# Performance work log

Measured on AMD Instinct MI355X. Metric: run time of the kernel, lower is better.

The kernel has to match this reference:

```python
import jax, jax.numpy as jnp
import numpy as np

E = 1024      # embed_dim
H = 16        # num_heads
HD = E // H   # head_dim = 64
M = 64        # num_landmarks


def setup_inputs() -> dict:
    key = jax.random.key(0)
    ks = jax.random.split(key, 9)
    B, Lq, Lk = 2, 2048, 2048
    inv = 1.0 / np.sqrt(E)
    return {
        "query": jax.random.normal(ks[0], (B, Lq, E), dtype=jnp.float32),
        "key":   jax.random.normal(ks[1], (B, Lk, E), dtype=jnp.float32),
        "value": jax.random.normal(ks[2], (B, Lk, E), dtype=jnp.float32),
        # learned params (xavier-ish scale)
        "Wv": jax.random.normal(ks[3], (E, E), dtype=jnp.float32) * inv,
        "bv": jnp.zeros((E,), dtype=jnp.float32),
        "Wl": jax.random.normal(ks[4], (M, E), dtype=jnp.float32) * inv,
        "bl": jnp.zeros((M,), dtype=jnp.float32),
        "Wo": jax.random.normal(ks[5], (E, E), dtype=jnp.float32) * inv,
        "bo": jnp.zeros((E,), dtype=jnp.float32),
    }


def reference(query, key, value, Wv, bv, Wl, bl, Wo, bo):
    B, Lq, _ = query.shape
    Lk = key.shape[1]
    # value projection -> [B, H, Lk, HD]
    v = (value @ Wv.T + bv).reshape(B, Lk, H, HD).transpose(0, 2, 1, 3)
    # landmark projections + softmax over landmark dim
    ql = jax.nn.softmax((query @ Wl.T + bl) / np.sqrt(M), axis=-1)  # [B, Lq, M]
    kl = jax.nn.softmax((key @ Wl.T + bl) / np.sqrt(M), axis=-1)    # [B, Lk, M]
    # landmark attention: [B, Lq, Lk], scaled by sqrt(head_dim), softmax over keys
    attn = jax.nn.softmax(
        jnp.einsum("bqm,bkm->bqk", ql, kl) / np.sqrt(HD), axis=-1)
    # apply shared attention across heads: [B, H, Lq, HD]
    out_h = jnp.einsum("bqk,bhkd->bhqd", attn, v)
    out = out_h.transpose(0, 2, 1, 3).reshape(B, Lq, E)
    return out @ Wo.T + bo
```

## Files before the change

kernel.cpp:

```cpp
#include <hip/hip_runtime.h>
#include <hip/hip_bf16.h>
#include <cstdint>

typedef unsigned short u16;
typedef __attribute__((ext_vector_type(8))) short short8;
typedef __attribute__((ext_vector_type(4))) float f32x4;
typedef __attribute__((ext_vector_type(4))) unsigned short us4;

__device__ __forceinline__ u16 f2bf(float f) {
    union { float f; unsigned int i; } v; v.f = f;
    unsigned int x = v.i;
    unsigned int r = x + 0x7fffu + ((x >> 16) & 1u);
    return (u16)(r >> 16);
}

enum { EPI_F32 = 0, EPI_BF16 = 1, EPI_EXP_RS = 3, EPI_F32_DIV_CB = 4, EPI_LMSM = 5 };

template <int BM, int BN, int EPI, bool AF32, bool BF32>
__device__ __forceinline__ void gemm_body(
    char* __restrict__ smem,
    const void* __restrict__ Ax, const void* __restrict__ A2x,
    const void* __restrict__ Bx, void* __restrict__ Cv,
    int M, int N, int K, long sA, long sB, long sC,
    const float* __restrict__ biasCol, float* __restrict__ rowScale, float expScale,
    int m0, int n0, int z)
{
    constexpr int BK = 64;
    constexpr int MFRAG = (BM + 31) / 32;
    constexpr int NFRAG = BN / 32;
    constexpr int AG = (BM + 31) / 32;
    constexpr int BG = BN / 32;
    constexpr int TBUF = (BM + BN) * BK;

    const int tid = threadIdx.x;
    const int lane = tid & 63;
    const int quad = lane >> 4;
    const int l15 = lane & 15;
    const int w = tid >> 6;
    const int wm = w >> 1, wn = w & 1;

    const int r8 = tid >> 3;
    const int cl = tid & 7;
    const int cg = ((cl ^ (r8 & 7)) * 8);

    const u16* ap[AG];
    const float* apf[AG];
    if constexpr (AF32) {
        const float* base = (const float*)Ax;
        long mr = m0;
        if (A2x != nullptr && m0 >= (M >> 1)) { base = (const float*)A2x; mr = m0 - (M >> 1); }
        const float* Afb = base + (long)z * sA + (long)mr * K;
#pragma unroll
        for (int j = 0; j < AG; ++j) apf[j] = Afb + (long)(j * 32 + r8) * K + cg;
    } else {
        const u16* Ab = (const u16*)Ax + (long)z * sA + (long)m0 * K;
#pragma unroll
        for (int j = 0; j < AG; ++j) ap[j] = Ab + (long)(j * 32 + r8) * K + cg;
    }
    const u16* bp[BG];
    const float* bpf[BG];
    if constexpr (BF32) {
        const float* Bfb = (const float*)Bx + (long)z * sB + (long)n0 * K;
#pragma unroll
        for (int j = 0; j < BG; ++j) bpf[j] = Bfb + (long)(j * 32 + r8) * K + cg;
    } else {
        const u16* Bb = (const u16*)Bx + (long)z * sB + (long)n0 * K;
#pragma unroll
        for (int j = 0; j < BG; ++j) bp[j] = Bb + (long)(j * 32 + r8) * K + cg;
    }

    f32x4 acc[MFRAG][NFRAG] = {};
    const int sw = l15 & 7;
    u16* const base16 = (u16*)smem;
    const int NT = K / BK;

    {
        u16* As = base16;
        u16* Bs = base16 + BM * BK;
        if constexpr (!AF32) {
#pragma unroll
            for (int j = 0; j < AG; ++j) {
                __builtin_amdgcn_global_load_lds(
                    (const __attribute__((address_space(1))) void*)(ap[j]),
                    (__attribute__((address_space(3))) void*)(&As[(j * 32 + r8) * BK + cl * 8]),
                    16, 0, 0);
                ap[j] += BK;
            }
        } else {
#pragma unroll
            for (int j = 0; j < AG; ++j) {
                const float4 u0 = *(const float4*)(apf[j]);
                const float4 u1 = *(const float4*)(apf[j] + 4);
                short8 o;
                o[0] = (short)f2bf(u0.x); o[1] = (short)f2bf(u0.y);
                o[2] = (short)f2bf(u0.z); o[3] = (short)f2bf(u0.w);
                o[4] = (short)f2bf(u1.x); o[5] = (short)f2bf(u1.y);
                o[6] = (short)f2bf(u1.z); o[7] = (short)f2bf(u1.w);
                *(short8*)&As[(j * 32 + r8) * BK + cl * 8] = o;
                apf[j] += BK;
            }
        }
        if constexpr (!BF32) {
#pragma unroll
            for (int j = 0; j < BG; ++j) {
                __builtin_amdgcn_global_load_lds(
                    (const __attribute__((address_space(1))) void*)(bp[j]),
                    (__attribute__((address_space(3))) void*)(&Bs[(j * 32 + r8) * BK + cl * 8]),
                    16, 0, 0);
                bp[j] += BK;
            }
        } else {
#pragma unroll
            for (int j = 0; j < BG; ++j) {
                const float4 u0 = *(const float4*)(bpf[j]);
                const float4 u1 = *(const float4*)(bpf[j] + 4);
                short8 o;
                o[0] = (short)f2bf(u0.x); o[1] = (short)f2bf(u0.y);
                o[2] = (short)f2bf(u0.z); o[3] = (short)f2bf(u0.w);
                o[4] = (short)f2bf(u1.x); o[5] = (short)f2bf(u1.y);
                o[6] = (short)f2bf(u1.z); o[7] = (short)f2bf(u1.w);
                *(short8*)&Bs[(j * 32 + r8) * BK + cl * 8] = o;
                bpf[j] += BK;
            }
        }
    }
    __syncthreads();

    for (int t = 0; t < NT; ++t) {
        u16* Asc = base16 + (t & 1) * TBUF;
        u16* Bsc = Asc + BM * BK;
        u16* Asn = base16 + ((t + 1) & 1) * TBUF;
        u16* Bsn = Asn + BM * BK;
        const bool pf = (t + 1 < NT);

        float4 ra[AG][2];
        float4 rb[BG][2];
        if (pf) {
            if constexpr (!AF32) {
#pragma unroll
                for (int j = 0; j < AG; ++j) {
                    __builtin_amdgcn_global_load_lds(
                        (const __attribute__((address_space(1))) void*)(ap[j]),
                        (__attribute__((address_space(3))) void*)(&Asn[(j * 32 + r8) * BK + cl * 8]),
                        16, 0, 0);
                    ap[j] += BK;
                }
            } else {
#pragma unroll
                for (int j = 0; j < AG; ++j) {
                    ra[j][0] = *(const float4*)(apf[j]);
                    ra[j][1] = *(const float4*)(apf[j] + 4);
                    apf[j] += BK;
                }
            }
            if constexpr (!BF32) {
#pragma unroll
                for (int j = 0; j < BG; ++j) {
                    __builtin_amdgcn_global_load_lds(
                        (const __attribute__((address_space(1))) void*)(bp[j]),
                        (__attribute__((address_space(3))) void*)(&Bsn[(j * 32 + r8) * BK + cl * 8]),
                        16, 0, 0);
                    bp[j] += BK;
                }
            } else {
#pragma unroll
                for (int j = 0; j < BG; ++j) {
                    rb[j][0] = *(const float4*)(bpf[j]);
                    rb[j][1] = *(const float4*)(bpf[j] + 4);
                    bpf[j] += BK;
                }
            }
        }

#pragma unroll
        for (int ks = 0; ks < 2; ++ks) {
            short8 af[MFRAG], bfr[NFRAG];
#pragma unroll
            for (int i = 0; i < MFRAG; ++i)
                af[i] = *(const short8*)&Asc[(wm * (BM / 2) + i * 16 + l15) * BK +
                                             (((ks * 4 + quad) ^ sw) * 8)];
#pragma unroll
            for (int i = 0; i < NFRAG; ++i)
                bfr[i] = *(const short8*)&Bsc[(wn * (BN / 2) + i * 16 + l15) * BK +
                                              (((ks * 4 + quad) ^ sw) * 8)];
#pragma unroll
            for (int i = 0; i < MFRAG; ++i)
#pragma unroll
                for (int jn = 0; jn < NFRAG; ++jn)
                    acc[i][jn] = __builtin_amdgcn_mfma_f32_16x16x32_bf16(af[i], bfr[jn], acc[i][jn], 0, 0, 0);
        }

        if (pf) {
            if constexpr (AF32) {
#pragma unroll
                for (int j = 0; j < AG; ++j) {
                    short8 o;
                    o[0] = (short)f2bf(ra[j][0].x); o[1] = (short)f2bf(ra[j][0].y);
                    o[2] = (short)f2bf(ra[j][0].z); o[3] = (short)f2bf(ra[j][0].w);
                    o[4] = (short)f2bf(ra[j][1].x); o[5] = (short)f2bf(ra[j][1].y);
                    o[6] = (short)f2bf(ra[j][1].z); o[7] = (short)f2bf(ra[j][1].w);
                    *(short8*)&Asn[(j * 32 + r8) * BK + cl * 8] = o;
                }
            }
            if constexpr (BF32) {
#pragma unroll
                for (int j = 0; j < BG; ++j) {
                    short8 o;
                    o[0] = (short)f2bf(rb[j][0].x); o[1] = (short)f2bf(rb[j][0].y);
                    o[2] = (short)f2bf(rb[j][0].z); o[3] = (short)f2bf(rb[j][0].w);
                    o[4] = (short)f2bf(rb[j][1].x); o[5] = (short)f2bf(rb[j][1].y);
                    o[6] = (short)f2bf(rb[j][1].z); o[7] = (short)f2bf(rb[j][1].w);
                    *(short8*)&Bsn[(j * 32 + r8) * BK + cl * 8] = o;
                }
            }
        }
        __syncthreads();
    }

    if constexpr (EPI == EPI_LMSM) {
        float* red = (float*)(base16 + 2 * TBUF);
        float ev[4][NFRAG];
#pragma unroll
        for (int r = 0; r < 4; ++r) {
            float s = 0.f;
#pragma unroll
            for (int jn = 0; jn < NFRAG; ++jn) {
                const int col = wn * (BN / 2) + jn * 16 + l15;
                float v = exp2f((acc[0][jn][r] + biasCol[col]) * expScale);
                ev[r][jn] = v; s += v;
            }
            s += __shfl_xor(s, 1); s += __shfl_xor(s, 2);
            s += __shfl_xor(s, 4); s += __shfl_xor(s, 8);
            if (l15 == 0) red[wn * BM + wm * 16 + quad * 4 + r] = s;
        }
        __syncthreads();
#pragma unroll
        for (int r = 0; r < 4; ++r) {
            const int mrow = wm * 16 + quad * 4 + r;
            const float inv = 1.0f / (red[mrow] + red[BM + mrow]);
            const long m = m0 + mrow;
#pragma unroll
            for (int jn = 0; jn < NFRAG; ++jn) {
                const int col = wn * (BN / 2) + jn * 16 + l15;
                ((u16*)Cv)[m * N + col] = f2bf(ev[r][jn] * inv);
            }
        }
        return;
    } else {
#pragma unroll
        for (int i = 0; i < MFRAG; ++i) {
            const int mb = m0 + wm * (BM / 2) + i * 16 + quad * 4;
#pragma unroll
            for (int r = 0; r < 4; ++r) {
                const int m = mb + r;
                float rin = 0.f;
                if constexpr (EPI == EPI_F32_DIV_CB) rin = 1.0f / rowScale[(long)z * M + m];
                float rowsum = 0.f;
#pragma unroll
                for (int jn = 0; jn < NFRAG; ++jn) {
                    const int col = n0 + wn * (BN / 2) + jn * 16 + l15;
                    float v = acc[i][jn][r];
                    if constexpr (EPI == EPI_EXP_RS) { v = exp2f(v * expScale); rowsum += v; }
                    if constexpr (EPI == EPI_F32_DIV_CB) v = v * rin + biasCol[col];
                    if constexpr (EPI == EPI_F32 || EPI == EPI_F32_DIV_CB)
                        ((float*)Cv)[(long)z * sC + (long)m * N + col] = v;
                    else
                        ((u16*)Cv)[(long)z * sC + (long)m * N + col] = f2bf(v);
                }
                if constexpr (EPI == EPI_EXP_RS) {
                    rowsum += __shfl_xor(rowsum, 1);
                    rowsum += __shfl_xor(rowsum, 2);
                    rowsum += __shfl_xor(rowsum, 4);
                    rowsum += __shfl_xor(rowsum, 8);
                    if (l15 == 0) atomicAdd(&rowScale[(long)z * M + m], rowsum);
                }
            }
        }
    }
}

__global__ void __launch_bounds__(256)
gemm6_pipe(const u16* __restrict__ Pm, const u16* __restrict__ Ut, float* __restrict__ out,
           const float* __restrict__ bocomb, const float* __restrict__ rsc)
{
    extern __shared__ char smem[];
    constexpr int BK = 64, NT = 32;
    constexpr int TB = (64 + 128) * BK;
    const int tid = threadIdx.x;
    const int lane = tid & 63;
    const int quad = lane >> 4;
    const int l15 = lane & 15;
    const int w = tid >> 6;
    const int wm = w >> 1, wn = w & 1;
    const int z = blockIdx.z;
    const int m0 = blockIdx.y * 64;
    const int n0 = blockIdx.x * 128;

    const int r8 = tid >> 3;
    const int cl = tid & 7;
    const int cg = ((cl ^ (r8 & 7)) * 8);

    const u16* ap[2];
    const u16* bp[4];
    const u16* Ab = Pm + (long)z * 4194304 + (long)m0 * 2048;
    const u16* Bb = Ut + (long)z * 2097152 + (long)n0 * 2048;
#pragma unroll
    for (int j = 0; j < 2; ++j) ap[j] = Ab + (long)(j * 32 + r8) * 2048 + cg;
#pragma unroll
    for (int j = 0; j < 4; ++j) bp[j] = Bb + (long)(j * 32 + r8) * 2048 + cg;

    u16* const base16 = (u16*)smem;
    auto stage = [&](int bi) {
        u16* As = base16 + bi * TB;
        u16* Bs = As + 64 * BK;
#pragma unroll
        for (int j = 0; j < 2; ++j) {
            __builtin_amdgcn_global_load_lds(
                (const __attribute__((address_space(1))) void*)(ap[j]),
                (__attribute__((address_space(3))) void*)(&As[(j * 32 + r8) * BK + cl * 8]),
                16, 0, 0);
            ap[j] += BK;
        }
#pragma unroll
        for (int j = 0; j < 4; ++j) {
            __builtin_amdgcn_global_load_lds(
                (const __attribute__((address_space(1))) void*)(bp[j]),
                (__attribute__((address_space(3))) void*)(&Bs[(j * 32 + r8) * BK + cl * 8]),
                16, 0, 0);
            bp[j] += BK;
        }
    };

    f32x4 acc[2][4] = {};
    const int sw = l15 & 7;

    stage(0);
    stage(1);
    asm volatile("s_waitcnt vmcnt(6)" ::: "memory");
    __builtin_amdgcn_s_barrier();
    __builtin_amdgcn_sched_barrier(0);

    int cur = 0;
    for (int t = 0; t < NT; ++t) {
        int pre = cur + 2; if (pre >= 3) pre -= 3;
        if (t + 2 < NT) stage(pre);

        u16* Asc = base16 + cur * TB;
        u16* Bsc = Asc + 64 * BK;
#pragma unroll
        for (int ks = 0; ks < 2; ++ks) {
            short8 af[2], bfr[4];
#pragma unroll
            for (int i = 0; i < 2; ++i)
                af[i] = *(const short8*)&Asc[(wm * 32 + i * 16 + l15) * BK +
                                             (((ks * 4 + quad) ^ sw) * 8)];
#pragma unroll
            for (int i = 0; i < 4; ++i)
                bfr[i] = *(const short8*)&Bsc[(wn * 64 + i * 16 + l15) * BK +
                                              (((ks * 4 + quad) ^ sw) * 8)];
#pragma unroll
            for (int i = 0; i < 2; ++i)
#pragma unroll
                for (int jn = 0; jn < 4; ++jn)
                    acc[i][jn] = __builtin_amdgcn_mfma_f32_16x16x32_bf16(af[i], bfr[jn], acc[i][jn], 0, 0, 0);
        }

        if (t + 2 < NT) {
            asm volatile("s_waitcnt vmcnt(6)" ::: "memory");
            __builtin_amdgcn_s_barrier();
            __builtin_amdgcn_sched_barrier(0);
        } else if (t + 1 < NT) {
            asm volatile("s_waitcnt vmcnt(0)" ::: "memory");
            __builtin_amdgcn_s_barrier();
            __builtin_amdgcn_sched_barrier(0);
        }
        cur += 1; if (cur == 3) cur = 0;
    }

#pragma unroll
    for (int i = 0; i < 2; ++i) {
        const int mb = m0 + wm * 32 + i * 16 + quad * 4;
#pragma unroll
        for (int r = 0; r < 4; ++r) {
            const int m = mb + r;
            const float rin = 1.0f / rsc[z * 2048 + m];
#pragma unroll
            for (int jn = 0; jn < 4; ++jn) {
                const int col = n0 + wn * 64 + jn * 16 + l15;
                out[(long)z * 2097152 + (long)m * 1024 + col] =
                    acc[i][jn][r] * rin + bocomb[col];
            }
        }
    }
}

__global__ void __launch_bounds__(256)
fused23(const float* __restrict__ query, const float* __restrict__ key,
        const float* __restrict__ Wl, u16* __restrict__ qlkl,
        const float* __restrict__ bl,
        const float* __restrict__ Wo, const u16* __restrict__ WvT, u16* __restrict__ Wov,
        const float* __restrict__ bv, const float* __restrict__ bo,
        float* __restrict__ rsc, float* __restrict__ bocomb)
{
    extern __shared__ char smem[];
    const int b = blockIdx.x;
    if (b < 256) {
        gemm_body<32, 64, EPI_LMSM, true, true>(smem, query, key, Wl, qlkl,
            8192, 64, 1024, 0, 0, 0, bl, nullptr, 0.18033688011112042f,
            b * 32, 0, 0);
    } else if (b < 512) {
        const int t = b - 256;
        gemm_body<64, 64, EPI_BF16, true, false>(smem, Wo, nullptr, WvT, Wov,
            1024, 1024, 1024, 0, 0, 0, nullptr, nullptr, 0.f,
            (t >> 4) * 64, (t & 15) * 64, 0);
    } else if (b < 768) {
        const int row = (b - 512) * 4 + (threadIdx.x >> 6);
        const int lane = threadIdx.x & 63;
        float s = 0.f;
#pragma unroll
        for (int i = 0; i < 16; ++i) s += Wo[(long)row * 1024 + i * 64 + lane] * bv[i * 64 + lane];
        for (int o = 32; o; o >>= 1) s += __shfl_xor(s, o, 64);
        if (lane == 0) bocomb[row] = bo[row] + s;
    } else {
        rsc[(b - 768) * 256 + threadIdx.x] = 0.f;
    }
}

__global__ void __launch_bounds__(256)
fused45(const u16* __restrict__ Wov, const float* __restrict__ value, u16* __restrict__ Ut,
        const u16* __restrict__ qlkl, u16* __restrict__ Pm, float* __restrict__ rsc)
{
    extern __shared__ char smem[];
    const int b = blockIdx.x;
    if (b < 512) {
        const int x = b & 31, y = (b >> 5) & 7, z = b >> 8;
        gemm_body<128, 64, EPI_BF16, false, true>(smem, Wov, nullptr, value, Ut,
            1024, 2048, 1024, 0, 2097152, 2097152, nullptr, nullptr, 0.f,
            y * 128, x * 64, z);
    } else {
        const int t = b - 512;
        const int x = t & 15, y = (t >> 4) & 15, z = t >> 8;
        gemm_body<128, 128, EPI_EXP_RS, false, false>(smem, qlkl, nullptr, qlkl + 262144, Pm,
            2048, 2048, 64, 131072, 131072, 4194304, nullptr, rsc, 0.18033688011112042f,
            y * 128, x * 128, z);
    }
}

__global__ void __launch_bounds__(256)
prep_wvt(const float* __restrict__ Wv, u16* __restrict__ WvT)
{
    __shared__ float t[64][65];
    const int bx = blockIdx.x & 15, by = blockIdx.x >> 4;
    const int tid = threadIdx.x;
#pragma unroll
    for (int p = 0; p < 16; ++p) {
        int idx = p * 256 + tid;
        int r = idx >> 6, c = idx & 63;
        t[r][c] = Wv[(long)(by * 64 + r) * 1024 + bx * 64 + c];
    }
    __syncthreads();
#pragma unroll
    for (int p = 0; p < 16; ++p) {
        int idx = p * 256 + tid;
        int c = idx >> 6, r = idx & 63;
        WvT[(long)(bx * 64 + c) * 1024 + by * 64 + r] = f2bf(t[r][c]);
    }
}

extern "C" void kernel_launch(void* const* d_in, const int* in_sizes, int n_in,
                              void* d_out, int out_size, void* d_ws, size_t ws_size,
                              hipStream_t stream)
{
    const float* query = (const float*)d_in[0];
    const float* key   = (const float*)d_in[1];
    const float* value = (const float*)d_in[2];
    const float* Wv    = (const float*)d_in[3];
    const float* bv    = (const float*)d_in[4];
    const float* Wl    = (const float*)d_in[5];
    const float* bl    = (const float*)d_in[6];
    const float* Wo    = (const float*)d_in[7];
    const float* bo    = (const float*)d_in[8];
    float* out = (float*)d_out;

    char* ws = (char*)d_ws;
    u16*   WvT    = (u16*)  (ws + 27394048);
    u16*   Wov    = (u16*)  (ws + 29491200);
    u16*   qlkl   = (u16*)  (ws + 31588352);
    u16*   Ut     = (u16*)  (ws + 32636928);
    u16*   Pm     = (u16*)  (ws + 41025536);
    float* rsc    = (float*)(ws + 57802752);
    float* bocomb = (float*)(ws + 57819136);

    static bool attr_done = false;
    if (!attr_done) {
        (void)hipFuncSetAttribute((const void*)gemm6_pipe,
                                  hipFuncAttributeMaxDynamicSharedMemorySize, 73728);
        attr_done = true;
    }

    prep_wvt<<<dim3(256), 256, 0, stream>>>(Wv, WvT);

    fused23<<<dim3(784), 256, 32768, stream>>>(query, key, Wl, qlkl, bl,
                                               Wo, WvT, Wov, bv, bo, rsc, bocomb);

    fused45<<<dim3(1024), 256, 49152, stream>>>(Wov, value, Ut, qlkl, Pm, rsc);

    gemm6_pipe<<<dim3(8, 32, 2), 256, 73728, stream>>>(Pm, Ut, out, bocomb, rsc);
}
```

Before: 166.2 us.

## Fuse landmark score exp into final GEMM, dropping materialized attention matrix

The final output GEMM now computes the exp'd landmark-attention tile on the fly from ql/kl fragments (K=64) for each 64-key step. It writes that tile to LDS as bf16 and multiplies it against the Ut tile, accumulating row sums locally instead of through atomics. This removes the 2x2048x2048 bf16 Pm write/read, the rsc zeroing and the atomics, and the separate fused45 kernel, at the cost of recomputing QK^T per N-tile (8x redundancy), extra barriers per iteration, and a shallower double-buffered pipeline. The Ut projection becomes its own launch.

```diff
diff --git a/kernel.cpp b/kernel.cpp
--- a/kernel.cpp
+++ b/kernel.cpp
@@ -279,13 +279,25 @@
     }
 }
 
+template <int BM, int BN, int EPI, bool AF32, bool BF32>
 __global__ void __launch_bounds__(256)
-gemm6_pipe(const u16* __restrict__ Pm, const u16* __restrict__ Ut, float* __restrict__ out,
-           const float* __restrict__ bocomb, const float* __restrict__ rsc)
+gemm_bt(const void* __restrict__ Ax, const void* __restrict__ A2x,
+        const void* __restrict__ Bx, void* __restrict__ Cv,
+        int M, int N, int K, long sA, long sB, long sC,
+        const float* __restrict__ biasCol, float* __restrict__ rowScale, float expScale)
 {
     extern __shared__ char smem[];
-    constexpr int BK = 64, NT = 32;
-    constexpr int TB = (64 + 128) * BK;
+    gemm_body<BM, BN, EPI, AF32, BF32>(smem, Ax, A2x, Bx, Cv, M, N, K, sA, sB, sC,
+                                       biasCol, rowScale, expScale,
+                                       blockIdx.y * BM, blockIdx.x * BN, blockIdx.z);
+}
+
+__global__ void __launch_bounds__(256)
+fused56(const u16* __restrict__ qlkl, const u16* __restrict__ Ut,
+        float* __restrict__ out, const float* __restrict__ bocomb)
+{
+    extern __shared__ char smem[];
+    constexpr float SC = 0.18033688011112042f;
     const int tid = threadIdx.x;
     const int lane = tid & 63;
     const int quad = lane >> 4;
@@ -299,91 +311,145 @@
     const int r8 = tid >> 3;
     const int cl = tid & 7;
     const int cg = ((cl ^ (r8 & 7)) * 8);
-
-    const u16* ap[2];
-    const u16* bp[4];
-    const u16* Ab = Pm + (long)z * 4194304 + (long)m0 * 2048;
-    const u16* Bb = Ut + (long)z * 2097152 + (long)n0 * 2048;
-#pragma unroll
-    for (int j = 0; j < 2; ++j) ap[j] = Ab + (long)(j * 32 + r8) * 2048 + cg;
-#pragma unroll
-    for (int j = 0; j < 4; ++j) bp[j] = Bb + (long)(j * 32 + r8) * 2048 + cg;
-
-    u16* const base16 = (u16*)smem;
+    const int sw = l15 & 7;
+
+    u16* const pb = (u16*)(smem + 49152);
+    float* const redf = (float*)(smem + 57344);
+
+    const u16* qz = qlkl + (long)z * 131072 + (long)m0 * 64;
+    short8 qf0a, qf0b, qf1a, qf1b;
+    qf0a = *(const short8*)(qz + (wm * 32 + l15) * 64 + quad * 8);
+    qf0b = *(const short8*)(qz + (wm * 32 + 16 + l15) * 64 + quad * 8);
+    qf1a = *(const short8*)(qz + (wm * 32 + l15) * 64 + (4 + quad) * 8);
+    qf1b = *(const short8*)(qz + (wm * 32 + 16 + l15) * 64 + (4 + quad) * 8);
+
+    const u16* kp[2];
+    const u16* up[4];
+    {
+        const u16* klz = qlkl + 262144 + (long)z * 131072;
+#pragma unroll
+        for (int j = 0; j < 2; ++j) kp[j] = klz + (long)(j * 32 + r8) * 64 + cg;
+        const u16* uz = Ut + (long)z * 2097152 + (long)n0 * 2048;
+#pragma unroll
+        for (int j = 0; j < 4; ++j) up[j] = uz + (long)(j * 32 + r8) * 2048 + cg;
+    }
+
     auto stage = [&](int bi) {
-        u16* As = base16 + bi * TB;
-        u16* Bs = As + 64 * BK;
+        char* bufn = smem + bi * 24576;
+        u16* kls = (u16*)bufn;
+        u16* us = (u16*)(bufn + 8192);
 #pragma unroll
         for (int j = 0; j < 2; ++j) {
             __builtin_amdgcn_global_load_lds(
-                (const __attribute__((address_space(1))) void*)(ap[j]),
-                (__attribute__((address_space(3))) void*)(&As[(j * 32 + r8) * BK + cl * 8]),
+                (const __attribute__((address_space(1))) void*)(kp[j]),
+                (__attribute__((address_space(3))) void*)(&kls[(j * 32 + r8) * 64 + cl * 8]),
                 16, 0, 0);
-            ap[j] += BK;
+            kp[j] += 4096;
         }
 #pragma unroll
         for (int j = 0; j < 4; ++j) {
             __builtin_amdgcn_global_load_lds(
-                (const __attribute__((address_space(1))) void*)(bp[j]),
-                (__attribute__((address_space(3))) void*)(&Bs[(j * 32 + r8) * BK + cl * 8]),
+                (const __attribute__((address_space(1))) void*)(up[j]),
+                (__attribute__((address_space(3))) void*)(&us[(j * 32 + r8) * 64 + cl * 8]),
                 16, 0, 0);
-            bp[j] += BK;
+            up[j] += 64;
         }
     };
 
     f32x4 acc[2][4] = {};
-    const int sw = l15 & 7;
+    float rs[2][4] = {};
 
     stage(0);
-    stage(1);
-    asm volatile("s_waitcnt vmcnt(6)" ::: "memory");
+    asm volatile("s_waitcnt vmcnt(0)" ::: "memory");
     __builtin_amdgcn_s_barrier();
     __builtin_amdgcn_sched_barrier(0);
 
-    int cur = 0;
-    for (int t = 0; t < NT; ++t) {
-        int pre = cur + 2; if (pre >= 3) pre -= 3;
-        if (t + 2 < NT) stage(pre);
-
-        u16* Asc = base16 + cur * TB;
-        u16* Bsc = Asc + 64 * BK;
+    for (int t = 0; t < 32; ++t) {
+        const int cur = t & 1;
+        if (t + 1 < 32) stage(cur ^ 1);
+
+        char* bufc = smem + cur * 24576;
+        u16* klc = (u16*)bufc;
+        u16* uc = (u16*)(bufc + 8192);
+
+        f32x4 pacc[2][2] = {};
 #pragma unroll
         for (int ks = 0; ks < 2; ++ks) {
-            short8 af[2], bfr[4];
+            short8 bk[2];
+#pragma unroll
+            for (int jn = 0; jn < 2; ++jn)
+                bk[jn] = *(const short8*)&klc[(wn * 32 + jn * 16 + l15) * 64 +
+                                              (((ks * 4 + quad) ^ sw) * 8)];
+            const short8 qa = ks ? qf1a : qf0a;
+            const short8 qb = ks ? qf1b : qf0b;
+#pragma unroll
+            for (int jn = 0; jn < 2; ++jn) {
+                pacc[0][jn] = __builtin_amdgcn_mfma_f32_16x16x32_bf16(qa, bk[jn], pacc[0][jn], 0, 0, 0);
+                pacc[1][jn] = __builtin_amdgcn_mfma_f32_16x16x32_bf16(qb, bk[jn], pacc[1][jn], 0, 0, 0);
+            }
+        }
+
+#pragma unroll
+        for (int i = 0; i < 2; ++i)
+#pragma unroll
+            for (int r = 0; r < 4; ++r) {
+                const int ml = wm * 32 + i * 16 + quad * 4 + r;
+                const int mb8 = ml & 7;
+#pragma unroll
+                for (int jn = 0; jn < 2; ++jn) {
+                    const int kl_ = wn * 32 + jn * 16 + l15;
+                    const float v = exp2f(pacc[i][jn][r] * SC);
+                    rs[i][r] += v;
+                    pb[ml * 64 + ((((kl_ >> 3) ^ mb8)) << 3) + (kl_ & 7)] = f2bf(v);
+                }
+            }
+
+        asm volatile("s_waitcnt lgkmcnt(0)" ::: "memory");
+        __builtin_amdgcn_s_barrier();
+        __builtin_amdgcn_sched_barrier(0);
+
+#pragma unroll
+        for (int ks = 0; ks < 2; ++ks) {
+            short8 pa[2], bu[4];
 #pragma unroll
             for (int i = 0; i < 2; ++i)
-                af[i] = *(const short8*)&Asc[(wm * 32 + i * 16 + l15) * BK +
+                pa[i] = *(const short8*)&pb[(wm * 32 + i * 16 + l15) * 64 +
+                                            (((ks * 4 + quad) ^ sw) * 8)];
+#pragma unroll
+            for (int jn = 0; jn < 4; ++jn)
+                bu[jn] = *(const short8*)&uc[(wn * 64 + jn * 16 + l15) * 64 +
                                              (((ks * 4 + quad) ^ sw) * 8)];
 #pragma unroll
-            for (int i = 0; i < 4; ++i)
-                bfr[i] = *(const short8*)&Bsc[(wn * 64 + i * 16 + l15) * BK +
-                                              (((ks * 4 + quad) ^ sw) * 8)];
-#pragma unroll
             for (int i = 0; i < 2; ++i)
 #pragma unroll
                 for (int jn = 0; jn < 4; ++jn)
-                    acc[i][jn] = __builtin_amdgcn_mfma_f32_16x16x32_bf16(af[i], bfr[jn], acc[i][jn], 0, 0, 0);
-        }
-
-        if (t + 2 < NT) {
-            asm volatile("s_waitcnt vmcnt(6)" ::: "memory");
-            __builtin_amdgcn_s_barrier();
-            __builtin_amdgcn_sched_barrier(0);
-        } else if (t + 1 < NT) {
-            asm volatile("s_waitcnt vmcnt(0)" ::: "memory");
-            __builtin_amdgcn_s_barrier();
-            __builtin_amdgcn_sched_barrier(0);
-        }
-        cur += 1; if (cur == 3) cur = 0;
-    }
+                    acc[i][jn] = __builtin_amdgcn_mfma_f32_16x16x32_bf16(pa[i], bu[jn], acc[i][jn], 0, 0, 0);
+        }
+
+        asm volatile("s_waitcnt vmcnt(0)" ::: "memory");
+        __builtin_amdgcn_s_barrier();
+        __builtin_amdgcn_sched_barrier(0);
+    }
+
+#pragma unroll
+    for (int i = 0; i < 2; ++i)
+#pragma unroll
+        for (int r = 0; r < 4; ++r) {
+            float s = rs[i][r];
+            s += __shfl_xor(s, 1); s += __shfl_xor(s, 2);
+            s += __shfl_xor(s, 4); s += __shfl_xor(s, 8);
+            if (l15 == 0) redf[wn * 64 + wm * 32 + i * 16 + quad * 4 + r] = s;
+        }
+    __syncthreads();
 
 #pragma unroll
     for (int i = 0; i < 2; ++i) {
         const int mb = m0 + wm * 32 + i * 16 + quad * 4;
 #pragma unroll
         for (int r = 0; r < 4; ++r) {
+            const int ml = wm * 32 + i * 16 + quad * 4 + r;
+            const float rin = 1.0f / (redf[ml] + redf[64 + ml]);
             const int m = mb + r;
-            const float rin = 1.0f / rsc[z * 2048 + m];
 #pragma unroll
             for (int jn = 0; jn < 4; ++jn) {
                 const int col = n0 + wn * 64 + jn * 16 + l15;
@@ -400,7 +466,7 @@
         const float* __restrict__ bl,
         const float* __restrict__ Wo, const u16* __restrict__ WvT, u16* __restrict__ Wov,
         const float* __restrict__ bv, const float* __restrict__ bo,
-        float* __restrict__ rsc, float* __restrict__ bocomb)
+        float* __restrict__ bocomb)
 {
     extern __shared__ char smem[];
     const int b = blockIdx.x;
@@ -413,7 +479,7 @@
         gemm_body<64, 64, EPI_BF16, true, false>(smem, Wo, nullptr, WvT, Wov,
             1024, 1024, 1024, 0, 0, 0, nullptr, nullptr, 0.f,
             (t >> 4) * 64, (t & 15) * 64, 0);
-    } else if (b < 768) {
+    } else {
         const int row = (b - 512) * 4 + (threadIdx.x >> 6);
         const int lane = threadIdx.x & 63;
         float s = 0.f;
@@ -421,28 +487,6 @@
         for (int i = 0; i < 16; ++i) s += Wo[(long)row * 1024 + i * 64 + lane] * bv[i * 64 + lane];
         for (int o = 32; o; o >>= 1) s += __shfl_xor(s, o, 64);
         if (lane == 0) bocomb[row] = bo[row] + s;
-    } else {
-        rsc[(b - 768) * 256 + threadIdx.x] = 0.f;
-    }
-}
-
-__global__ void __launch_bounds__(256)
-fused45(const u16* __restrict__ Wov, const float* __restrict__ value, u16* __restrict__ Ut,
-        const u16* __restrict__ qlkl, u16* __restrict__ Pm, float* __restrict__ rsc)
-{
-    extern __shared__ char smem[];
-    const int b = blockIdx.x;
-    if (b < 512) {
-        const int x = b & 31, y = (b >> 5) & 7, z = b >> 8;
-        gemm_body<128, 64, EPI_BF16, false, true>(smem, Wov, nullptr, value, Ut,
-            1024, 2048, 1024, 0, 2097152, 2097152, nullptr, nullptr, 0.f,
-            y * 128, x * 64, z);
-    } else {
-        const int t = b - 512;
-        const int x = t & 15, y = (t >> 4) & 15, z = t >> 8;
-        gemm_body<128, 128, EPI_EXP_RS, false, false>(smem, qlkl, nullptr, qlkl + 262144, Pm,
-            2048, 2048, 64, 131072, 131072, 4194304, nullptr, rsc, 0.18033688011112042f,
-            y * 128, x * 128, z);
     }
 }
 
@@ -487,23 +531,16 @@
     u16*   Wov    = (u16*)  (ws + 29491200);
     u16*   qlkl   = (u16*)  (ws + 31588352);
     u16*   Ut     = (u16*)  (ws + 32636928);
-    u16*   Pm     = (u16*)  (ws + 41025536);
-    float* rsc    = (float*)(ws + 57802752);
     float* bocomb = (float*)(ws + 57819136);
 
-    static bool attr_done = false;
-    if (!attr_done) {
-        (void)hipFuncSetAttribute((const void*)gemm6_pipe,
-                                  hipFuncAttributeMaxDynamicSharedMemorySize, 73728);
-        attr_done = true;
-    }
-
     prep_wvt<<<dim3(256), 256, 0, stream>>>(Wv, WvT);
 
-    fused23<<<dim3(784), 256, 32768, stream>>>(query, key, Wl, qlkl, bl,
-                                               Wo, WvT, Wov, bv, bo, rsc, bocomb);
-
-    fused45<<<dim3(1024), 256, 49152, stream>>>(Wov, value, Ut, qlkl, Pm, rsc);
-
-    gemm6_pipe<<<dim3(8, 32, 2), 256, 73728, stream>>>(Pm, Ut, out, bocomb, rsc);
-}
+    fused23<<<dim3(768), 256, 32768, stream>>>(query, key, Wl, qlkl, bl,
+                                               Wo, WvT, Wov, bv, bo, bocomb);
+
+    gemm_bt<128, 64, EPI_BF16, false, true><<<dim3(32, 8, 2), 256, 49152, stream>>>(
+        Wov, nullptr, value, Ut, 1024, 2048, 1024, 0, 2097152, 2097152,
+        nullptr, nullptr, 0.f);
+
+    fused56<<<dim3(8, 32, 2), 256, 57856, stream>>>(qlkl, Ut, out, bocomb);
+}
```

Result: slower. 191.1 us (+15.0%).

## Split final GEMM tile across eight waves with double-buffered LDS

Applied to the files above, without the earlier changes.

The final GEMM (attention probabilities times projected values) now runs 512 threads per 64x128 tile instead of 256. Each of the eight waves computes a 32x32 sub-tile instead of 32x64, which halves the accumulators per wave. The three-stage LDS pipeline with manual vmcnt waits is replaced by a two-stage double buffer with __syncthreads, cutting shared memory to 48KB. The aim is more waves to hide latency, at the cost of more LDS fragment reloads per MFMA and a shallower prefetch.

```diff
diff --git a/kernel.cpp b/kernel.cpp
--- a/kernel.cpp
+++ b/kernel.cpp
@@ -279,9 +279,9 @@
     }
 }
 
-__global__ void __launch_bounds__(256)
-gemm6_pipe(const u16* __restrict__ Pm, const u16* __restrict__ Ut, float* __restrict__ out,
-           const float* __restrict__ bocomb, const float* __restrict__ rsc)
+__global__ void __launch_bounds__(512)
+gemm6_512(const u16* __restrict__ Pm, const u16* __restrict__ Ut, float* __restrict__ out,
+          const float* __restrict__ bocomb, const float* __restrict__ rsc)
 {
     extern __shared__ char smem[];
     constexpr int BK = 64, NT = 32;
@@ -291,7 +291,7 @@
     const int quad = lane >> 4;
     const int l15 = lane & 15;
     const int w = tid >> 6;
-    const int wm = w >> 1, wn = w & 1;
+    const int wm = w & 1, wn = w >> 1;
     const int z = blockIdx.z;
     const int m0 = blockIdx.y * 64;
     const int n0 = blockIdx.x * 128;
@@ -299,82 +299,61 @@
     const int r8 = tid >> 3;
     const int cl = tid & 7;
     const int cg = ((cl ^ (r8 & 7)) * 8);
-
-    const u16* ap[2];
-    const u16* bp[4];
-    const u16* Ab = Pm + (long)z * 4194304 + (long)m0 * 2048;
-    const u16* Bb = Ut + (long)z * 2097152 + (long)n0 * 2048;
-#pragma unroll
-    for (int j = 0; j < 2; ++j) ap[j] = Ab + (long)(j * 32 + r8) * 2048 + cg;
-#pragma unroll
-    for (int j = 0; j < 4; ++j) bp[j] = Bb + (long)(j * 32 + r8) * 2048 + cg;
+    const int sw = l15 & 7;
+
+    const u16* ap = Pm + (long)z * 4194304 + (long)(m0 + r8) * 2048 + cg;
+    const u16* bp[2];
+#pragma unroll
+    for (int j = 0; j < 2; ++j)
+        bp[j] = Ut + (long)z * 2097152 + (long)(n0 + j * 64 + r8) * 2048 + cg;
 
     u16* const base16 = (u16*)smem;
     auto stage = [&](int bi) {
         u16* As = base16 + bi * TB;
         u16* Bs = As + 64 * BK;
+        __builtin_amdgcn_global_load_lds(
+            (const __attribute__((address_space(1))) void*)(ap),
+            (__attribute__((address_space(3))) void*)(&As[r8 * BK + cl * 8]),
+            16, 0, 0);
+        ap += BK;
 #pragma unroll
         for (int j = 0; j < 2; ++j) {
             __builtin_amdgcn_global_load_lds(
-                (const __attribute__((address_space(1))) void*)(ap[j]),
-                (__attribute__((address_space(3))) void*)(&As[(j * 32 + r8) * BK + cl * 8]),
-                16, 0, 0);
-            ap[j] += BK;
-        }
-#pragma unroll
-        for (int j = 0; j < 4; ++j) {
-            __builtin_amdgcn_global_load_lds(
                 (const __attribute__((address_space(1))) void*)(bp[j]),
-                (__attribute__((address_space(3))) void*)(&Bs[(j * 32 + r8) * BK + cl * 8]),
+                (__attribute__((address_space(3))) void*)(&Bs[(j * 64 + r8) * BK + cl * 8]),
                 16, 0, 0);
             bp[j] += BK;
         }
     };
 
-    f32x4 acc[2][4] = {};
-    const int sw = l15 & 7;
+    f32x4 acc[2][2] = {};
 
     stage(0);
-    stage(1);
-    asm volatile("s_waitcnt vmcnt(6)" ::: "memory");
-    __builtin_amdgcn_s_barrier();
-    __builtin_amdgcn_sched_barrier(0);
-
-    int cur = 0;
+    __syncthreads();
+
     for (int t = 0; t < NT; ++t) {
-        int pre = cur + 2; if (pre >= 3) pre -= 3;
-        if (t + 2 < NT) stage(pre);
-
-        u16* Asc = base16 + cur * TB;
+        u16* Asc = base16 + (t & 1) * TB;
         u16* Bsc = Asc + 64 * BK;
+        if (t + 1 < NT) stage((t + 1) & 1);
+
 #pragma unroll
         for (int ks = 0; ks < 2; ++ks) {
-            short8 af[2], bfr[4];
+            short8 af[2], bu[2];
 #pragma unroll
             for (int i = 0; i < 2; ++i)
                 af[i] = *(const short8*)&Asc[(wm * 32 + i * 16 + l15) * BK +
                                              (((ks * 4 + quad) ^ sw) * 8)];
 #pragma unroll
-            for (int i = 0; i < 4; ++i)
-                bfr[i] = *(const short8*)&Bsc[(wn * 64 + i * 16 + l15) * BK +
+            for (int jn = 0; jn < 2; ++jn)
+                bu[jn] = *(const short8*)&Bsc[(wn * 32 + jn * 16 + l15) * BK +
                                               (((ks * 4 + quad) ^ sw) * 8)];
 #pragma unroll
             for (int i = 0; i < 2; ++i)
 #pragma unroll
-                for (int jn = 0; jn < 4; ++jn)
-                    acc[i][jn] = __builtin_amdgcn_mfma_f32_16x16x32_bf16(af[i], bfr[jn], acc[i][jn], 0, 0, 0);
-        }
-
-        if (t + 2 < NT) {
-            asm volatile("s_waitcnt vmcnt(6)" ::: "memory");
-            __builtin_amdgcn_s_barrier();
-            __builtin_amdgcn_sched_barrier(0);
-        } else if (t + 1 < NT) {
-            asm volatile("s_waitcnt vmcnt(0)" ::: "memory");
-            __builtin_amdgcn_s_barrier();
-            __builtin_amdgcn_sched_barrier(0);
-        }
-        cur += 1; if (cur == 3) cur = 0;
+                for (int jn = 0; jn < 2; ++jn)
+                    acc[i][jn] = __builtin_amdgcn_mfma_f32_16x16x32_bf16(af[i], bu[jn], acc[i][jn], 0, 0, 0);
+        }
+        __syncthreads();
     }
 
 #pragma unroll
@@ -385,8 +364,8 @@
             const int m = mb + r;
             const float rin = 1.0f / rsc[z * 2048 + m];
 #pragma unroll
-            for (int jn = 0; jn < 4; ++jn) {
-                const int col = n0 + wn * 64 + jn * 16 + l15;
+            for (int jn = 0; jn < 2; ++jn) {
+                const int col = n0 + wn * 32 + jn * 16 + l15;
                 out[(long)z * 2097152 + (long)m * 1024 + col] =
                     acc[i][jn][r] * rin + bocomb[col];
             }
@@ -491,13 +470,6 @@
     float* rsc    = (float*)(ws + 57802752);
     float* bocomb = (float*)(ws + 57819136);
 
-    static bool attr_done = false;
-    if (!attr_done) {
-        (void)hipFuncSetAttribute((const void*)gemm6_pipe,
-                                  hipFuncAttributeMaxDynamicSharedMemorySize, 73728);
-        attr_done = true;
-    }
-
     prep_wvt<<<dim3(256), 256, 0, stream>>>(Wv, WvT);
 
     fused23<<<dim3(784), 256, 32768, stream>>>(query, key, Wl, qlkl, bl,
@@ -505,5 +477,5 @@
 
     fused45<<<dim3(1024), 256, 49152, stream>>>(Wov, value, Ut, qlkl, Pm, rsc);
 
-    gemm6_pipe<<<dim3(8, 32, 2), 256, 73728, stream>>>(Pm, Ut, out, bocomb, rsc);
-}
+    gemm6_512<<<dim3(8, 32, 2), 512, 49152, stream>>>(Pm, Ut, out, bocomb, rsc);
+}
```

Result: no change. 168.4 us (+1.3%).
